# Optimization experiments

Hardware: AMD Instinct MI355X
Metric: run time of the kernel (lower is better)

The kernel has to match this reference:

```python
import jax, jax.numpy as jnp
import numpy as np

DIM = 1024
DFF = 4096
LN_EPS = 1e-5


def _layernorm(x, g, b):
    mu = jnp.mean(x, axis=-1, keepdims=True)
    var = jnp.mean((x - mu) ** 2, axis=-1, keepdims=True)
    return (x - mu) * jax.lax.rsqrt(var + LN_EPS) * g + b


def setup_inputs() -> dict:
    key = jax.random.key(0)
    ks = jax.random.split(key, 16)
    B, L, D, F = 4, 2048, DIM, DFF
    return {
        "x": jax.random.normal(ks[0], (B, L, D), dtype=jnp.float32),
        "hidden_real": jax.random.normal(ks[1], (B, D), dtype=jnp.float32),
        "hidden_imag": jax.random.normal(ks[2], (B, D), dtype=jnp.float32),
        # SConvLayer params (real/imag pairs, mirroring torch.view_as_real storage)
        "phazor_init": jax.random.normal(ks[3], (D, 2), dtype=jnp.float32),
        "phazor": jax.random.normal(ks[4], (D, 2), dtype=jnp.float32),
        # fc (gate) linear
        "fc_w": jax.random.normal(ks[5], (D, D), dtype=jnp.float32) / np.sqrt(D),
        "fc_b": jax.random.normal(ks[6], (D,), dtype=jnp.float32) * 0.01,
        # FFN
        "w1": jax.random.normal(ks[7], (F, D), dtype=jnp.float32) / np.sqrt(D),
        "b1": jax.random.normal(ks[8], (F,), dtype=jnp.float32) * 0.01,
        "w2": jax.random.normal(ks[9], (D, F), dtype=jnp.float32) / np.sqrt(F),
        "b2": jax.random.normal(ks[10], (D,), dtype=jnp.float32) * 0.01,
        # shared LayerNorm (used twice in the block with the same params)
        "ln_g": jnp.ones((D,), dtype=jnp.float32),
        "ln_b": jnp.zeros((D,), dtype=jnp.float32),
    }


def reference(x, hidden_real, hidden_imag, phazor_init, phazor,
              fc_w, fc_b, w1, b1, w2, b2, ln_g, ln_b):
    B, L, D = x.shape
    hidden = (hidden_real + 1j * hidden_imag).astype(jnp.complex64)

    x_res = x
    xn = _layernorm(x, ln_g, ln_b)

    # --- SConvLayer ---
    pz = (phazor[:, 0] + 1j * phazor[:, 1]).astype(jnp.complex64)  # [D]
    # magnitude exp(-|z|^2), phase = angle(z)
    p = jnp.exp(-(pz.real ** 2 + pz.imag ** 2)) * jnp.exp(1j * jnp.angle(pz))
    t = jnp.arange(L)
    prog = p[None, :] ** t[:, None]                      # [L, D] complex
    init_c = (phazor_init[:, 0] + 1j * phazor_init[:, 1]).astype(jnp.complex64)
    filt = prog * init_c[None, :]                        # [L, D]
    n2 = 2 * L
    filt_fft = jnp.fft.fft(filt, n=n2, axis=0)           # [2L, D]
    x_fft = jnp.fft.fft(xn.astype(jnp.complex64), n=n2, axis=1)  # [B, 2L, D]
    conv = jnp.fft.ifft(filt_fft[None] * x_fft, axis=1)[:, :L]   # [B, L, D]
    conv_with_past = conv + hidden[:, None, :] * prog[None] * p[None, None, :]
    sx = conv_with_past.real

    # --- gate ---
    y = jax.nn.silu(jnp.einsum('bld,ed->ble', x_res, fc_w) + fc_b)
    x2 = sx * y + x_res

    # --- FFN (same LayerNorm params) ---
    x3 = _layernorm(x2, ln_g, ln_b)
    h = jax.nn.silu(jnp.einsum('bld,fd->blf', x3, w1) + b1)
    out = jnp.einsum('blf,df->bld', h, w2) + b2 + x2
    return out, conv_with_past
```

## Files before the change

### kernel.cpp

```cpp
#include <hip/hip_runtime.h>
#include <hip/hip_bf16.h>

#define D_MODEL 1024
#define D_FF    4096
#define SEQ_LEN 2048
#define NBATCH  4
#define NROWS   (NBATCH*SEQ_LEN)
#define NCHUNK  32
#define CHUNK_L (SEQ_LEN/NCHUNK)
#define LN_EPS  1e-5f

typedef __hip_bfloat16 bf16;
typedef __attribute__((ext_vector_type(8))) short bf16x8;
typedef __attribute__((ext_vector_type(4))) float f32x4;

__device__ __forceinline__ void gload16(const bf16* g, bf16* l) {
    __builtin_amdgcn_global_load_lds(
        (const __attribute__((address_space(1))) void*)g,
        (__attribute__((address_space(3))) void*)l, 16, 0, 0);
}

__global__ void cast4(const float4* __restrict__ in, ushort4* __restrict__ out, int n4) {
    int i = blockIdx.x * blockDim.x + threadIdx.x;
    if (i < n4) {
        float4 v = in[i];
        union { ushort4 u; bf16 b[4]; } cv;
        cv.b[0] = __float2bfloat16(v.x); cv.b[1] = __float2bfloat16(v.y);
        cv.b[2] = __float2bfloat16(v.z); cv.b[3] = __float2bfloat16(v.w);
        out[i] = cv.u;
    }
}

__global__ void compute_pvec(const float* __restrict__ phz, float* __restrict__ pv) {
    int d = blockIdx.x * blockDim.x + threadIdx.x;
    if (d >= D_MODEL) return;
    float re = phz[2*d], im = phz[2*d+1];
    float r2 = re*re + im*im;
    float mag = expf(-r2);
    float pr, pim;
    if (r2 > 0.f) { float inv = mag / sqrtf(r2); pr = re*inv; pim = im*inv; }
    else          { pr = mag; pim = 0.f; }
    float ar = pr, ai = pim;
    #pragma unroll
    for (int i = 0; i < 6; i++) { float nr = ar*ar - ai*ai; float ni = 2.f*ar*ai; ar = nr; ai = ni; }
    pv[d]            = pr;
    pv[D_MODEL+d]    = pim;
    pv[2*D_MODEL+d]  = ar;
    pv[3*D_MODEL+d]  = ai;
}

__global__ __launch_bounds__(256) void ln_fused(const float* __restrict__ x,
                                                const float* __restrict__ g,
                                                const float* __restrict__ bta,
                                                float* __restrict__ outf,
                                                bf16*  __restrict__ outb,
                                                bf16*  __restrict__ rawb)
{
    int row = blockIdx.x;
    int tid = threadIdx.x;
    const float4* xr = (const float4*)(x + (size_t)row * D_MODEL);
    float4 v = xr[tid];
    if (rawb) {
        union { ushort4 u; bf16 b[4]; } cv;
        cv.b[0]=__float2bfloat16(v.x); cv.b[1]=__float2bfloat16(v.y);
        cv.b[2]=__float2bfloat16(v.z); cv.b[3]=__float2bfloat16(v.w);
        ((ushort4*)(rawb + (size_t)row * D_MODEL))[tid] = cv.u;
    }
    float s  = v.x + v.y + v.z + v.w;
    float s2 = v.x*v.x + v.y*v.y + v.z*v.z + v.w*v.w;
    for (int off = 32; off; off >>= 1) { s += __shfl_down(s, off); s2 += __shfl_down(s2, off); }
    __shared__ float red[8];
    int wid = tid >> 6, lane = tid & 63;
    if (lane == 0) { red[wid] = s; red[4+wid] = s2; }
    __syncthreads();
    if (tid == 0) {
        red[0] = red[0]+red[1]+red[2]+red[3];
        red[4] = red[4]+red[5]+red[6]+red[7];
    }
    __syncthreads();
    float mu  = red[0] * (1.f/D_MODEL);
    float var = red[4] * (1.f/D_MODEL) - mu*mu;
    float rstd = rsqrtf(var + LN_EPS);
    float4 gv = ((const float4*)g)[tid];
    float4 bv = ((const float4*)bta)[tid];
    float4 o;
    o.x = (v.x-mu)*rstd*gv.x + bv.x;
    o.y = (v.y-mu)*rstd*gv.y + bv.y;
    o.z = (v.z-mu)*rstd*gv.z + bv.z;
    o.w = (v.w-mu)*rstd*gv.w + bv.w;
    if (outf) ((float4*)(outf + (size_t)row * D_MODEL))[tid] = o;
    if (outb) {
        union { ushort4 u; bf16 b[4]; } cv;
        cv.b[0]=__float2bfloat16(o.x); cv.b[1]=__float2bfloat16(o.y);
        cv.b[2]=__float2bfloat16(o.z); cv.b[3]=__float2bfloat16(o.w);
        ((ushort4*)(outb + (size_t)row * D_MODEL))[tid] = cv.u;
    }
}

__global__ __launch_bounds__(256) void gate_ln(const float* __restrict__ cwp, int cstride,
                                               const bf16*  __restrict__ y,
                                               const float* __restrict__ x,
                                               const float* __restrict__ g,
                                               const float* __restrict__ bta,
                                               float* __restrict__ x2,
                                               bf16*  __restrict__ x3b)
{
    int row = blockIdx.x;
    int tid = threadIdx.x;
    size_t base = (size_t)row * D_MODEL + tid*4;
    float4 xv = *(const float4*)(x + base);
    union { ushort4 u; bf16 b[4]; } yv;
    yv.u = *(const ushort4*)(y + base);
    float4 cw;
    if (cstride == 1) {
        cw = *(const float4*)(cwp + base);
    } else {
        const float2* cp = (const float2*)cwp + base;
        cw.x = cp[0].x; cw.y = cp[1].x; cw.z = cp[2].x; cw.w = cp[3].x;
    }
    float4 v;
    v.x = cw.x * __bfloat162float(yv.b[0]) + xv.x;
    v.y = cw.y * __bfloat162float(yv.b[1]) + xv.y;
    v.z = cw.z * __bfloat162float(yv.b[2]) + xv.z;
    v.w = cw.w * __bfloat162float(yv.b[3]) + xv.w;
    *(float4*)(x2 + base) = v;

    float s  = v.x + v.y + v.z + v.w;
    float s2 = v.x*v.x + v.y*v.y + v.z*v.z + v.w*v.w;
    for (int off = 32; off; off >>= 1) { s += __shfl_down(s, off); s2 += __shfl_down(s2, off); }
    __shared__ float red[8];
    int wid = tid >> 6, lane = tid & 63;
    if (lane == 0) { red[wid] = s; red[4+wid] = s2; }
    __syncthreads();
    if (tid == 0) {
        red[0] = red[0]+red[1]+red[2]+red[3];
        red[4] = red[4]+red[5]+red[6]+red[7];
    }
    __syncthreads();
    float mu  = red[0] * (1.f/D_MODEL);
    float var = red[4] * (1.f/D_MODEL) - mu*mu;
    float rstd = rsqrtf(var + LN_EPS);
    float4 gv = ((const float4*)g)[tid];
    float4 bv = ((const float4*)bta)[tid];
    union { ushort4 u; bf16 b[4]; } cv;
    cv.b[0] = __float2bfloat16((v.x-mu)*rstd*gv.x + bv.x);
    cv.b[1] = __float2bfloat16((v.y-mu)*rstd*gv.y + bv.y);
    cv.b[2] = __float2bfloat16((v.z-mu)*rstd*gv.z + bv.z);
    cv.b[3] = __float2bfloat16((v.w-mu)*rstd*gv.w + bv.w);
    *(ushort4*)(x3b + base) = cv.u;
}

__global__ __launch_bounds__(256) void scan_pass1(const float* __restrict__ xn,
                                                  const float* __restrict__ pv,
                                                  const float* __restrict__ pini,
                                                  float* __restrict__ Sc)
{
    int d = blockIdx.x * 256 + threadIdx.x;
    int c = blockIdx.y, b = blockIdx.z;
    float pr = pv[d], pim = pv[D_MODEL+d];
    float icr = pini[2*d], ici = pini[2*d+1];
    float Sr = 0.f, Si = 0.f;
    const float* xp = xn + ((size_t)b*SEQ_LEN + c*CHUNK_L) * D_MODEL + d;
    #pragma unroll 8
    for (int i = 0; i < CHUNK_L; i++) {
        float xv = xp[(size_t)i * D_MODEL];
        float nr = pr*Sr - pim*Si + icr*xv;
        float ni = pr*Si + pim*Sr + ici*xv;
        Sr = nr; Si = ni;
    }
    size_t o = ((size_t)b*NCHUNK + c) * D_MODEL + d;
    Sc[2*o] = Sr; Sc[2*o+1] = Si;
}

__global__ __launch_bounds__(256) void scan_prefix(const float* __restrict__ Sc,
                                                   const float* __restrict__ pv,
                                                   const float* __restrict__ hr,
                                                   const float* __restrict__ hi,
                                                   float* __restrict__ pref)
{
    int d = blockIdx.x * 256 + threadIdx.x;
    int b = blockIdx.y;
    float qr = pv[2*D_MODEL+d], qi = pv[3*D_MODEL+d];
    float Ur = hr[b*D_MODEL+d], Ui = hi[b*D_MODEL+d];
    for (int c = 0; c < NCHUNK; c++) {
        size_t o = ((size_t)b*NCHUNK + c) * D_MODEL + d;
        pref[2*o] = Ur; pref[2*o+1] = Ui;
        float sr = Sc[2*o], si = Sc[2*o+1];
        float nr = qr*Ur - qi*Ui + sr;
        float ni = qr*Ui + qi*Ur + si;
        Ur = nr; Ui = ni;
    }
}

__global__ __launch_bounds__(256) void scan_pass2(const float* __restrict__ xn,
                                                  const float* __restrict__ pv,
                                                  const float* __restrict__ pini,
                                                  const float* __restrict__ pref,
                                                  float* __restrict__ cwp,
                                                  int interleaved)
{
    int d = blockIdx.x * 256 + threadIdx.x;
    int c = blockIdx.y, b = blockIdx.z;
    float pr = pv[d], pim = pv[D_MODEL+d];
    float icr = pini[2*d], ici = pini[2*d+1];
    size_t po = ((size_t)b*NCHUNK + c) * D_MODEL + d;
    float Ur = pref[2*po], Ui = pref[2*po+1];
    size_t base = ((size_t)b*SEQ_LEN + c*CHUNK_L) * D_MODEL + d;
    const float* xp = xn + base;
    if (interleaved) {
        float2* cp = (float2*)cwp + base;
        #pragma unroll 8
        for (int i = 0; i < CHUNK_L; i++) {
            float xv = xp[(size_t)i * D_MODEL];
            float nr = pr*Ur - pim*Ui + icr*xv;
            float ni = pr*Ui + pim*Ur + ici*xv;
            Ur = nr; Ui = ni;
            cp[(size_t)i * D_MODEL] = make_float2(Ur, Ui);
        }
    } else {
        float* cp = cwp + base;
        #pragma unroll 8
        for (int i = 0; i < CHUNK_L; i++) {
            float xv = xp[(size_t)i * D_MODEL];
            float nr = pr*Ur - pim*Ui + icr*xv;
            float ni = pr*Ui + pim*Ur + ici*xv;
            Ur = nr; Ui = ni;
            cp[(size_t)i * D_MODEL] = Ur;
        }
    }
}

template<int EPI>
__device__ __forceinline__ void epi_store(float v, size_t idx,
                                          const float* e0, int e0_stride, const float* e1,
                                          float* outf, bf16* outb)
{
    if (EPI == 1) {
        float yv = v / (1.f + __expf(-v));
        outb[idx] = __float2bfloat16(yv);
    } else {
        outf[idx] = v + e0[idx];
    }
}

#define BM 128
#define BN 128
#define BK 32

template<int EPI>
__global__ __launch_bounds__(256) void gemm_bt(const bf16* __restrict__ A,
                                               const bf16* __restrict__ Bt,
                                               const float* __restrict__ bias,
                                               const float* __restrict__ e0, int e0_stride,
                                               const float* __restrict__ e1,
                                               float* __restrict__ outf,
                                               bf16*  __restrict__ outb,
                                               int M, int N, int K)
{
    __shared__ __align__(16) bf16 As[3][BM*BK];
    __shared__ __align__(16) bf16 Bs[3][BM*BK];
    int tid = threadIdx.x;
    int m0 = blockIdx.x * BM;
    int n0 = blockIdx.y * BN;

    int wid = tid >> 6, lane = tid & 63;
    int wm = (wid >> 1) * 64, wn = (wid & 1) * 64;
    int lr = lane & 15;
    int lkc = lane >> 4;

    int rl = lane >> 2;
    int cS = (lane & 3) ^ ((rl >> 1) & 3);
    const bf16* gA0 = A  + (size_t)(m0 +      wid*16 + rl) * K + cS*8;
    const bf16* gA1 = A  + (size_t)(m0 + 64 + wid*16 + rl) * K + cS*8;
    const bf16* gB0 = Bt + (size_t)(n0 +      wid*16 + rl) * K + cS*8;
    const bf16* gB1 = Bt + (size_t)(n0 + 64 + wid*16 + rl) * K + cS*8;
    int lo0 = (     wid*16) * BK;
    int lo1 = (64 + wid*16) * BK;

    int keyr = (lr >> 1) & 3;
    int cR = (lkc ^ keyr) * 8;
    int offA[4], offB[4];
    #pragma unroll
    for (int i = 0; i < 4; i++) {
        offA[i] = (wm + i*16 + lr) * BK + cR;
        offB[i] = (wn + i*16 + lr) * BK + cR;
    }

    int nt = K / BK;
    auto stA = [&](int slot, int tile) {
        int k0 = tile * BK;
        gload16(gA0 + k0, &As[slot][lo0]);
        gload16(gA1 + k0, &As[slot][lo1]);
    };
    auto stB = [&](int slot, int tile) {
        int k0 = tile * BK;
        gload16(gB0 + k0, &Bs[slot][lo0]);
        gload16(gB1 + k0, &Bs[slot][lo1]);
    };

    f32x4 acc[4][4] = {};
    stA(0, 0); stB(0, 0); stA(1, 1); stB(1, 1); stB(2, 2);

    int s = 0;
    for (int t = 0; t < nt; ++t) {
        int sA = (s >= 1) ? s - 1 : 2;
        if (t < nt - 2)       { asm volatile("s_waitcnt vmcnt(6)" ::: "memory"); }
        else if (t == nt - 2) { asm volatile("s_waitcnt vmcnt(4)" ::: "memory"); }
        else                  { asm volatile("s_waitcnt vmcnt(0)" ::: "memory"); }
        __builtin_amdgcn_s_barrier();
        asm volatile("" ::: "memory");
        bf16x8 af0[2], bfv[4];
        #pragma unroll
        for (int i = 0; i < 2; i++) af0[i] = *(const bf16x8*)&As[s][offA[i]];
        #pragma unroll
        for (int j = 0; j < 4; j++) bfv[j] = *(const bf16x8*)&Bs[s][offB[j]];
        if (t + 2 < nt) stA(sA, t + 2);
        asm volatile("s_waitcnt lgkmcnt(0)" ::: "memory");
        __builtin_amdgcn_sched_barrier(0);
        __builtin_amdgcn_s_setprio(1);
        #pragma unroll
        for (int i = 0; i < 2; i++)
            #pragma unroll
            for (int j = 0; j < 4; j++)
                acc[i][j] = __builtin_amdgcn_mfma_f32_16x16x32_bf16(af0[i], bfv[j], acc[i][j], 0, 0, 0);
        __builtin_amdgcn_s_setprio(0);
        __builtin_amdgcn_s_barrier();
        asm volatile("" ::: "memory");
        bf16x8 af1[2];
        #pragma unroll
        for (int i = 0; i < 2; i++) af1[i] = *(const bf16x8*)&As[s][offA[2+i]];
        if (t + 3 < nt) stB(s, t + 3);
        asm volatile("s_waitcnt lgkmcnt(0)" ::: "memory");
        __builtin_amdgcn_sched_barrier(0);
        __builtin_amdgcn_s_setprio(1);
        #pragma unroll
        for (int i = 0; i < 2; i++)
            #pragma unroll
            for (int j = 0; j < 4; j++)
                acc[2+i][j] = __builtin_amdgcn_mfma_f32_16x16x32_bf16(af1[i], bfv[j], acc[2+i][j], 0, 0, 0);
        __builtin_amdgcn_s_setprio(0);
        s = (s == 2) ? 0 : s + 1;
    }
    asm volatile("s_waitcnt vmcnt(0)" ::: "memory");

    int mrow = 4 * (lane >> 4);
    #pragma unroll
    for (int i = 0; i < 4; i++) {
        #pragma unroll
        for (int j = 0; j < 4; j++) {
            int nb = n0 + wn + j*16 + lr;
            float bb = bias[nb];
            #pragma unroll
            for (int r = 0; r < 4; r++) {
                int m = m0 + wm + i*16 + mrow + r;
                size_t idx = (size_t)m * N + nb;
                epi_store<EPI>(acc[i][j][r] + bb, idx, e0, e0_stride, e1, outf, outb);
            }
        }
    }
}

#define TM 256
#define TN 256

template<int EPI>
__global__ __launch_bounds__(512, 2) void gemm256p(const bf16* __restrict__ A,
                                                   const bf16* __restrict__ Bt,
                                                   const float* __restrict__ bias,
                                                   const float* __restrict__ e0, int e0_stride,
                                                   const float* __restrict__ e1,
                                                   float* __restrict__ outf,
                                                   bf16*  __restrict__ outb,
                                                   int M, int N, int K)
{
    __shared__ __align__(16) bf16 As[3][TM*BK];
    __shared__ __align__(16) bf16 Bs[3][TN*BK];
    int tid = threadIdx.x;
    int m0 = blockIdx.x * TM;
    int n0 = blockIdx.y * TN;

    int wid = tid >> 6, lane = tid & 63;
    int wr = wid >> 2, wc = wid & 3;
    int wm = wr * 128, wn = wc * 64;
    int lr = lane & 15;
    int lkc = lane >> 4;

    int rs = tid >> 2;
    int cS = (tid & 3) ^ ((rs >> 1) & 3);
    const bf16* gA = A  + (size_t)m0 * K + cS*8;
    const bf16* gB = Bt + (size_t)n0 * K + cS*8;
    int ldst = tid * 8;

    int keyr = (lr >> 1) & 3;
    int cR = (lkc ^ keyr) * 8;
    int offA[8], offB[4];
    #pragma unroll
    for (int i = 0; i < 8; i++) offA[i] = (wm + i*16 + lr) * BK + cR;
    #pragma unroll
    for (int j = 0; j < 4; j++) offB[j] = (wn + j*16 + lr) * BK + cR;

    int nt = K / BK;
    auto stA = [&](int slot, int tile) {
        int k0 = tile * BK;
        gload16(gA + (size_t)rs * K + k0,         &As[slot][ldst]);
        gload16(gA + (size_t)(128 + rs) * K + k0, &As[slot][4096 + ldst]);
    };
    auto stB = [&](int slot, int tile) {
        int k0 = tile * BK;
        gload16(gB + (size_t)rs * K + k0,         &Bs[slot][ldst]);
        gload16(gB + (size_t)(128 + rs) * K + k0, &Bs[slot][4096 + ldst]);
    };

    f32x4 acc[8][4] = {};
    stA(0, 0); stB(0, 0); stA(1, 1); stB(1, 1); stB(2, 2);

    int s = 0;
    for (int t = 0; t < nt; ++t) {
        int sA = (s >= 1) ? s - 1 : 2;
        if (t < nt - 2)       { asm volatile("s_waitcnt vmcnt(6)" ::: "memory"); }
        else if (t == nt - 2) { asm volatile("s_waitcnt vmcnt(4)" ::: "memory"); }
        else                  { asm volatile("s_waitcnt vmcnt(0)" ::: "memory"); }
        __builtin_amdgcn_s_barrier();
        asm volatile("" ::: "memory");
        bf16x8 af0[4], bfv[4];
        #pragma unroll
        for (int i = 0; i < 4; i++) af0[i] = *(const bf16x8*)&As[s][offA[i]];
        #pragma unroll
        for (int j = 0; j < 4; j++) bfv[j] = *(const bf16x8*)&Bs[s][offB[j]];
        if (t + 2 < nt) stA(sA, t + 2);
        asm volatile("s_waitcnt lgkmcnt(0)" ::: "memory");
        __builtin_amdgcn_sched_barrier(0);
        __builtin_amdgcn_s_setprio(1);
        #pragma unroll
        for (int i = 0; i < 4; i++)
            #pragma unroll
            for (int j = 0; j < 4; j++)
                acc[i][j] = __builtin_amdgcn_mfma_f32_16x16x32_bf16(af0[i], bfv[j], acc[i][j], 0, 0, 0);
        __builtin_amdgcn_s_setprio(0);
        __builtin_amdgcn_s_barrier();
        asm volatile("" ::: "memory");
        bf16x8 af1[4];
        #pragma unroll
        for (int i = 0; i < 4; i++) af1[i] = *(const bf16x8*)&As[s][offA[4+i]];
        if (t + 3 < nt) stB(s, t + 3);
        asm volatile("s_waitcnt lgkmcnt(0)" ::: "memory");
        __builtin_amdgcn_sched_barrier(0);
        __builtin_amdgcn_s_setprio(1);
        #pragma unroll
        for (int i = 0; i < 4; i++)
            #pragma unroll
            for (int j = 0; j < 4; j++)
                acc[4+i][j] = __builtin_amdgcn_mfma_f32_16x16x32_bf16(af1[i], bfv[j], acc[4+i][j], 0, 0, 0);
        __builtin_amdgcn_s_setprio(0);
        s = (s == 2) ? 0 : s + 1;
    }
    asm volatile("s_waitcnt vmcnt(0)" ::: "memory");

    int mrow = 4 * (lane >> 4);
    #pragma unroll
    for (int i = 0; i < 8; i++) {
        #pragma unroll
        for (int j = 0; j < 4; j++) {
            int nb = n0 + wn + j*16 + lr;
            float bb = bias[nb];
            #pragma unroll
            for (int r = 0; r < 4; r++) {
                int m = m0 + wm + i*16 + mrow + r;
                size_t idx = (size_t)m * N + nb;
                epi_store<EPI>(acc[i][j][r] + bb, idx, e0, e0_stride, e1, outf, outb);
            }
        }
    }
}

extern "C" void kernel_launch(void* const* d_in, const int* in_sizes, int n_in,
                              void* d_out, int out_size, void* d_ws, size_t ws_size,
                              hipStream_t stream)
{
    const float* x    = (const float*)d_in[0];
    const float* hr   = (const float*)d_in[1];
    const float* hi   = (const float*)d_in[2];
    const float* pini = (const float*)d_in[3];
    const float* phz  = (const float*)d_in[4];
    const float* fcw  = (const float*)d_in[5];
    const float* fcb  = (const float*)d_in[6];
    const float* w1   = (const float*)d_in[7];
    const float* b1   = (const float*)d_in[8];
    const float* w2   = (const float*)d_in[9];
    const float* b2   = (const float*)d_in[10];
    const float* lng  = (const float*)d_in[11];
    const float* lnb  = (const float*)d_in[12];

    float* out = (float*)d_out;
    float* cwp = out + (size_t)NROWS * D_MODEL;
    int interleaved = (out_size >= NROWS * D_MODEL * 3) ? 1 : 0;

    char* ws = (char*)d_ws;
    size_t off = 0;
    bf16*  wfcb = (bf16*)(ws + off);  off += (size_t)D_MODEL*D_MODEL*2;
    bf16*  w1b  = (bf16*)(ws + off);  off += (size_t)D_FF*D_MODEL*2;
    bf16*  w2b  = (bf16*)(ws + off);  off += (size_t)D_MODEL*D_FF*2;
    float* pv   = (float*)(ws + off); off += (size_t)4*D_MODEL*4;
    float* xn   = (float*)(ws + off); off += (size_t)NROWS*D_MODEL*4;
    bf16*  xbf  = (bf16*)(ws + off);  off += (size_t)NROWS*D_MODEL*2;
    float* Sc   = (float*)(ws + off); off += (size_t)NBATCH*NCHUNK*D_MODEL*2*4;
    float* pref = (float*)(ws + off); off += (size_t)NBATCH*NCHUNK*D_MODEL*2*4;
    float* x2   = (float*)(ws + off); off += (size_t)NROWS*D_MODEL*4;
    bf16*  x3b  = (bf16*)(ws + off);  off += (size_t)NROWS*D_MODEL*2;
    bf16*  hbuf = (bf16*)(ws + off);  off += (size_t)NROWS*D_FF*2;
    bf16*  ybuf = (bf16*)(ws + off);  off += (size_t)NROWS*D_MODEL*2;

    cast4<<<1024, 256, 0, stream>>>((const float4*)fcw, (ushort4*)wfcb, D_MODEL*D_MODEL/4);
    cast4<<<4096, 256, 0, stream>>>((const float4*)w1,  (ushort4*)w1b,  D_FF*D_MODEL/4);
    cast4<<<4096, 256, 0, stream>>>((const float4*)w2,  (ushort4*)w2b,  D_MODEL*D_FF/4);

    compute_pvec<<<4, 256, 0, stream>>>(phz, pv);

    ln_fused<<<NROWS, 256, 0, stream>>>(x, lng, lnb, xn, nullptr, xbf);

    scan_pass1<<<dim3(4, NCHUNK, NBATCH), 256, 0, stream>>>(xn, pv, pini, Sc);
    scan_prefix<<<dim3(4, NBATCH), 256, 0, stream>>>(Sc, pv, hr, hi, pref);
    scan_pass2<<<dim3(4, NCHUNK, NBATCH), 256, 0, stream>>>(xn, pv, pini, pref, cwp, interleaved);

    gemm_bt<1><<<dim3(NROWS/BM, D_MODEL/BN), 256, 0, stream>>>(
        xbf, wfcb, fcb, nullptr, 1, nullptr, nullptr, ybuf, NROWS, D_MODEL, D_MODEL);

    gate_ln<<<NROWS, 256, 0, stream>>>(cwp, interleaved ? 2 : 1, ybuf, x, lng, lnb, x2, x3b);

    gemm256p<1><<<dim3(NROWS/TM, D_FF/TN), 512, 0, stream>>>(
        x3b, w1b, b1, nullptr, 1, nullptr, nullptr, hbuf, NROWS, D_FF, D_MODEL);

    gemm_bt<2><<<dim3(NROWS/BM, D_MODEL/BN), 256, 0, stream>>>(
        hbuf, w2b, b2, x2, 1, nullptr, out, nullptr, NROWS, D_MODEL, D_FF);
}
```

Before: 284.3 us.

## Replace 128x128 GEMM with 512-thread 128x256 tile kernel for fc and w2

Replaces the 256-thread 128x128 gemm_bt with a 512-thread gemmA using 128x256 output tiles (8 waves in a 2x4 grid), applied to both the fc gate GEMM and the w2 down-projection. The A and B prefetch now run at the same depth of two tiles ahead through a shared slot, with simpler vmcnt waits. The wider tile raises B reuse and halves the block count, but uses more LDS per block (about 72 KB). With 256 blocks on a large-CU GPU this may lower occupancy and load balance.

```diff
diff --git a/kernel.cpp b/kernel.cpp
--- a/kernel.cpp
+++ b/kernel.cpp
@@ -243,39 +243,37 @@
     }
 }
 
-#define BM 128
-#define BN 128
 #define BK 32
 
+#define TM2 128
+#define TN2 256
+
 template<int EPI>
-__global__ __launch_bounds__(256) void gemm_bt(const bf16* __restrict__ A,
-                                               const bf16* __restrict__ Bt,
-                                               const float* __restrict__ bias,
-                                               const float* __restrict__ e0, int e0_stride,
-                                               const float* __restrict__ e1,
-                                               float* __restrict__ outf,
-                                               bf16*  __restrict__ outb,
-                                               int M, int N, int K)
-{
-    __shared__ __align__(16) bf16 As[3][BM*BK];
-    __shared__ __align__(16) bf16 Bs[3][BM*BK];
+__global__ __launch_bounds__(512) void gemmA(const bf16* __restrict__ A,
+                                             const bf16* __restrict__ Bt,
+                                             const float* __restrict__ bias,
+                                             const float* __restrict__ e0,
+                                             float* __restrict__ outf,
+                                             bf16*  __restrict__ outb,
+                                             int M, int N, int K)
+{
+    __shared__ __align__(16) bf16 As[3][TM2*BK];
+    __shared__ __align__(16) bf16 Bs[3][TN2*BK];
     int tid = threadIdx.x;
-    int m0 = blockIdx.x * BM;
-    int n0 = blockIdx.y * BN;
+    int m0 = blockIdx.x * TM2;
+    int n0 = blockIdx.y * TN2;
 
     int wid = tid >> 6, lane = tid & 63;
-    int wm = (wid >> 1) * 64, wn = (wid & 1) * 64;
+    int wr = wid >> 2, wc = wid & 3;
+    int wm = wr * 64, wn = wc * 64;
     int lr = lane & 15;
     int lkc = lane >> 4;
 
-    int rl = lane >> 2;
-    int cS = (lane & 3) ^ ((rl >> 1) & 3);
-    const bf16* gA0 = A  + (size_t)(m0 +      wid*16 + rl) * K + cS*8;
-    const bf16* gA1 = A  + (size_t)(m0 + 64 + wid*16 + rl) * K + cS*8;
-    const bf16* gB0 = Bt + (size_t)(n0 +      wid*16 + rl) * K + cS*8;
-    const bf16* gB1 = Bt + (size_t)(n0 + 64 + wid*16 + rl) * K + cS*8;
-    int lo0 = (     wid*16) * BK;
-    int lo1 = (64 + wid*16) * BK;
+    int rs = tid >> 2;
+    int cS = (tid & 3) ^ ((rs >> 1) & 3);
+    const bf16* gA = A  + (size_t)m0 * K + cS*8;
+    const bf16* gB = Bt + (size_t)n0 * K + cS*8;
+    int ldst = tid * 8;
 
     int keyr = (lr >> 1) & 3;
     int cR = (lkc ^ keyr) * 8;
@@ -289,24 +287,22 @@
     int nt = K / BK;
     auto stA = [&](int slot, int tile) {
         int k0 = tile * BK;
-        gload16(gA0 + k0, &As[slot][lo0]);
-        gload16(gA1 + k0, &As[slot][lo1]);
+        gload16(gA + (size_t)rs * K + k0, &As[slot][ldst]);
     };
     auto stB = [&](int slot, int tile) {
         int k0 = tile * BK;
-        gload16(gB0 + k0, &Bs[slot][lo0]);
-        gload16(gB1 + k0, &Bs[slot][lo1]);
+        gload16(gB + (size_t)rs * K + k0,         &Bs[slot][ldst]);
+        gload16(gB + (size_t)(128 + rs) * K + k0, &Bs[slot][4096 + ldst]);
     };
 
     f32x4 acc[4][4] = {};
-    stA(0, 0); stB(0, 0); stA(1, 1); stB(1, 1); stB(2, 2);
+    stA(0, 0); stB(0, 0); stA(1, 1); stB(1, 1);
 
     int s = 0;
     for (int t = 0; t < nt; ++t) {
-        int sA = (s >= 1) ? s - 1 : 2;
-        if (t < nt - 2)       { asm volatile("s_waitcnt vmcnt(6)" ::: "memory"); }
-        else if (t == nt - 2) { asm volatile("s_waitcnt vmcnt(4)" ::: "memory"); }
-        else                  { asm volatile("s_waitcnt vmcnt(0)" ::: "memory"); }
+        int sN = (s >= 1) ? s - 1 : 2;
+        if (t < nt - 1) { asm volatile("s_waitcnt vmcnt(3)" ::: "memory"); }
+        else            { asm volatile("s_waitcnt vmcnt(0)" ::: "memory"); }
         __builtin_amdgcn_s_barrier();
         asm volatile("" ::: "memory");
         bf16x8 af0[2], bfv[4];
@@ -314,7 +310,7 @@
         for (int i = 0; i < 2; i++) af0[i] = *(const bf16x8*)&As[s][offA[i]];
         #pragma unroll
         for (int j = 0; j < 4; j++) bfv[j] = *(const bf16x8*)&Bs[s][offB[j]];
-        if (t + 2 < nt) stA(sA, t + 2);
+        if (t + 2 < nt) stA(sN, t + 2);
         asm volatile("s_waitcnt lgkmcnt(0)" ::: "memory");
         __builtin_amdgcn_sched_barrier(0);
         __builtin_amdgcn_s_setprio(1);
@@ -329,7 +325,7 @@
         bf16x8 af1[2];
         #pragma unroll
         for (int i = 0; i < 2; i++) af1[i] = *(const bf16x8*)&As[s][offA[2+i]];
-        if (t + 3 < nt) stB(s, t + 3);
+        if (t + 2 < nt) stB(sN, t + 2);
         asm volatile("s_waitcnt lgkmcnt(0)" ::: "memory");
         __builtin_amdgcn_sched_barrier(0);
         __builtin_amdgcn_s_setprio(1);
@@ -354,7 +350,7 @@
             for (int r = 0; r < 4; r++) {
                 int m = m0 + wm + i*16 + mrow + r;
                 size_t idx = (size_t)m * N + nb;
-                epi_store<EPI>(acc[i][j][r] + bb, idx, e0, e0_stride, e1, outf, outb);
+                epi_store<EPI>(acc[i][j][r] + bb, idx, e0, 1, nullptr, outf, outb);
             }
         }
     }
@@ -522,14 +518,14 @@
     scan_prefix<<<dim3(4, NBATCH), 256, 0, stream>>>(Sc, pv, hr, hi, pref);
     scan_pass2<<<dim3(4, NCHUNK, NBATCH), 256, 0, stream>>>(xn, pv, pini, pref, cwp, interleaved);
 
-    gemm_bt<1><<<dim3(NROWS/BM, D_MODEL/BN), 256, 0, stream>>>(
-        xbf, wfcb, fcb, nullptr, 1, nullptr, nullptr, ybuf, NROWS, D_MODEL, D_MODEL);
+    gemmA<1><<<dim3(NROWS/TM2, D_MODEL/TN2), 512, 0, stream>>>(
+        xbf, wfcb, fcb, nullptr, nullptr, ybuf, NROWS, D_MODEL, D_MODEL);
 
     gate_ln<<<NROWS, 256, 0, stream>>>(cwp, interleaved ? 2 : 1, ybuf, x, lng, lnb, x2, x3b);
 
     gemm256p<1><<<dim3(NROWS/TM, D_FF/TN), 512, 0, stream>>>(
         x3b, w1b, b1, nullptr, 1, nullptr, nullptr, hbuf, NROWS, D_FF, D_MODEL);
 
-    gemm_bt<2><<<dim3(NROWS/BM, D_MODEL/BN), 256, 0, stream>>>(
-        hbuf, w2b, b2, x2, 1, nullptr, out, nullptr, NROWS, D_MODEL, D_FF);
-}
+    gemmA<2><<<dim3(NROWS/TM2, D_MODEL/TN2), 512, 0, stream>>>(
+        hbuf, w2b, b2, x2, out, nullptr, NROWS, D_MODEL, D_FF);
+}
```

New measurement: 288.7 us. About the same (+1.6%).
